# Kernel optimization log

Hardware: AMD Instinct MI355X
Metric: run time of the kernel (lower is better)

## Reference

```python
import jax, jax.numpy as jnp
import numpy as np

GRID = 4
N = GRID * GRID  # 16 nodes
CIN = 16
HID = 64
HEADS = 4
OUT = 256
NEG_SLOPE = 0.2  # PyG GATConv default leaky relu slope
LN_EPS = 1e-5


def _adj_mask():
    # 4-connected grid adjacency + self loops (PyG GATConv add_self_loops=True)
    m = np.zeros((N, N), dtype=bool)
    for i in range(GRID):
        for j in range(GRID):
            u = i * GRID + j
            if j + 1 < GRID:
                v = i * GRID + j + 1
                m[u, v] = m[v, u] = True
            if i + 1 < GRID:
                v = (i + 1) * GRID + j
                m[u, v] = m[v, u] = True
    np.fill_diagonal(m, True)
    return m

ADJ = jnp.asarray(_adj_mask())  # [N, N], adj[i, j] = j is a (self-)neighbor of i


def gat_layer(h, W, a_src, a_dst, b, concat):
    """PyG GATConv on the fixed grid graph, dense-masked form.
    h: [B, N, Fin]; W: [Fin, HEADS*C]; a_src/a_dst: [HEADS, C]."""
    B = h.shape[0]
    H, C = a_src.shape
    wh = (h @ W).reshape(B, N, H, C)                       # [B, N, H, C]
    e_src = jnp.einsum('bnhc,hc->bnh', wh, a_src)          # alpha_src . Wh_j
    e_dst = jnp.einsum('bnhc,hc->bnh', wh, a_dst)          # alpha_dst . Wh_i
    # score[b, i, j, h]: target i attends to source j
    e = e_dst[:, :, None, :] + e_src[:, None, :, :]
    e = jax.nn.leaky_relu(e, NEG_SLOPE)
    e = jnp.where(ADJ[None, :, :, None], e, -1e9)
    alpha = jax.nn.softmax(e, axis=2)                      # softmax over sources j
    out = jnp.einsum('bijh,bjhc->bihc', alpha, wh)         # [B, N, H, C]
    if concat:
        out = out.reshape(B, N, H * C)
    else:
        out = out.mean(axis=2)
    return out + b


def setup_inputs() -> dict:
    key = jax.random.key(0)
    ks = jax.random.split(key, 24)
    s = 0.05
    B = 16384
    inp = {
        'x': jax.random.normal(ks[0], (B, CIN, GRID, GRID), dtype=jnp.float32),
        'w_in': jax.random.normal(ks[1], (CIN, HID), dtype=jnp.float32) * s,
        'b_in': jnp.zeros((HID,), jnp.float32),
        # GAT layer 0: in 64 -> 4 heads x 64, concat
        'W0': jax.random.normal(ks[2], (HID, HEADS * HID), dtype=jnp.float32) * s,
        'asrc0': jax.random.normal(ks[3], (HEADS, HID), dtype=jnp.float32) * s,
        'adst0': jax.random.normal(ks[4], (HEADS, HID), dtype=jnp.float32) * s,
        'bb0': jnp.zeros((HEADS * HID,), jnp.float32),
        # GAT layer 1: in 256 -> 4 heads x 64, concat
        'W1': jax.random.normal(ks[5], (HEADS * HID, HEADS * HID), dtype=jnp.float32) * s,
        'asrc1': jax.random.normal(ks[6], (HEADS, HID), dtype=jnp.float32) * s,
        'adst1': jax.random.normal(ks[7], (HEADS, HID), dtype=jnp.float32) * s,
        'bb1': jnp.zeros((HEADS * HID,), jnp.float32),
        # GAT layer 2: in 256 -> 4 heads x 64, mean over heads (concat=False)
        'W2': jax.random.normal(ks[8], (HEADS * HID, HEADS * HID), dtype=jnp.float32) * s,
        'asrc2': jax.random.normal(ks[9], (HEADS, HID), dtype=jnp.float32) * s,
        'adst2': jax.random.normal(ks[10], (HEADS, HID), dtype=jnp.float32) * s,
        'bb2': jnp.zeros((HID,), jnp.float32),
        # output MLP: 64 -> 128 (LN, ReLU) -> 256
        'w1': jax.random.normal(ks[11], (HID, OUT // 2), dtype=jnp.float32) * s,
        'b1': jnp.zeros((OUT // 2,), jnp.float32),
        'ln_g': jnp.ones((OUT // 2,), jnp.float32),
        'ln_b': jnp.zeros((OUT // 2,), jnp.float32),
        'w2': jax.random.normal(ks[12], (OUT // 2, OUT), dtype=jnp.float32) * s,
        'b2': jnp.zeros((OUT,), jnp.float32),
    }
    return inp


def reference(x, w_in, b_in, W0, asrc0, adst0, bb0, W1, asrc1, adst1, bb1,
              W2, asrc2, adst2, bb2, w1, b1, ln_g, ln_b, w2, b2):
    B = x.shape[0]
    # grid_to_graph: (B, C, H, W) -> (B, N, C) node features
    h = jnp.transpose(x, (0, 2, 3, 1)).reshape(B, N, CIN)
    h = jax.nn.relu(h @ w_in + b_in)
    h = gat_layer(h, W0, asrc0, adst0, bb0, concat=True)
    h = jax.nn.relu(h)  # dropout is identity at inference
    h = gat_layer(h, W1, asrc1, adst1, bb1, concat=True)
    h = jax.nn.relu(h)
    h = gat_layer(h, W2, asrc2, adst2, bb2, concat=False)  # [B, N, 64]
    g = h.mean(axis=1)  # global_mean_pool over the 16 nodes of each graph
    # MLP with LayerNorm
    y = g @ w1 + b1
    mu = y.mean(axis=-1, keepdims=True)
    var = ((y - mu) ** 2).mean(axis=-1, keepdims=True)
    y = (y - mu) * jax.lax.rsqrt(var + LN_EPS) * ln_g + ln_b
    y = jax.nn.relu(y)
    return y @ w2 + b2
```

## Files before the change

### kernel.cpp

```cpp
#include <hip/hip_runtime.h>
#include <hip/hip_bf16.h>

typedef short s8v __attribute__((ext_vector_type(8)));
typedef short s4v __attribute__((ext_vector_type(4)));
typedef float f4v __attribute__((ext_vector_type(4)));

#define WSTR 36
#define AP   20

#define HIXBASE(s, quad) (((s)*4 + (quad))*256)

__device__ constexpr unsigned KMASK[16] = {
  0x0013u,0x0027u,0x004Eu,0x008Cu,
  0x0131u,0x0272u,0x04E4u,0x08C8u,
  0x1310u,0x2720u,0x4E40u,0x8C80u,
  0x3100u,0x7200u,0xE400u,0xC800u};

__device__ __forceinline__ short f2b(float x){
  __hip_bfloat16 h = __float2bfloat16(x);
  return *reinterpret_cast<short*>(&h);
}
__device__ __forceinline__ float b2f(short s){
  __hip_bfloat16 h = *reinterpret_cast<__hip_bfloat16*>(&s);
  return __bfloat162float(h);
}
__device__ __forceinline__ unsigned pk2(float a, float b){
  unsigned ua = __float_as_uint(a), ub = __float_as_uint(b);
  ua += 0x7fffu + ((ua >> 16) & 1u);
  ub += 0x7fffu + ((ub >> 16) & 1u);
  return __builtin_amdgcn_perm(ub, ua, 0x07060302);
}

__global__ __launch_bounds__(256) void prep_all(
  const float* __restrict__ W0, const float* __restrict__ as0, const float* __restrict__ ad0,
  const float* __restrict__ W1, const float* __restrict__ as1, const float* __restrict__ ad1,
  const float* __restrict__ W2, const float* __restrict__ as2, const float* __restrict__ ad2,
  const float* __restrict__ w_in,
  short* __restrict__ ws)
{
  short* WPin = ws;
  short* WP0  = ws + 2048;
  short* WP1  = ws + 2048 + 17408;
  short* WP2  = ws + 2048 + 17408 + 69632;

  const int t = threadIdx.x, l = t & 63;
  const int gid = blockIdx.x*4 + (t >> 6);

  if (gid < 288){
    const float* W; short* WP; int u = gid, f, s, KS;
    if (u < 32)      { W = W0; WP = WP0; KS = 2; f = u >> 1; s = u & 1; }
    else if (u < 160){ u -= 32;  W = W1; WP = WP1; KS = 8; f = u >> 3; s = u & 7; }
    else             { u -= 160; W = W2; WP = WP2; KS = 8; f = u >> 3; s = u & 7; }
    const int lq = l & 15, quad = l >> 4;
    union { s8v v; short s16[8]; } o;
    #pragma unroll
    for (int j = 0; j < 8; ++j)
      o.s16[j] = f2b(W[(s*32 + quad*8 + j)*256 + f*16 + lq]);
    *(s8v*)(WP + ((f*KS + s)*64 + l)*8) = o.v;
  } else if (gid < 292){
    const int f = gid - 288;
    const int lq = l & 15, quad = l >> 4;
    union { s8v v; short s16[8]; } o;
    #pragma unroll
    for (int j = 0; j < 8; ++j){
      const int k = quad*8 + j;
      o.s16[j] = (k < 16) ? f2b(w_in[k*64 + f*16 + lq]) : (short)0;
    }
    *(s8v*)(WPin + (f*64 + l)*8) = o.v;
  } else {
    int u = gid - 292;
    const float* W; const float* as; const float* ad; short* WP; int KS, k;
    if (u < 64)      { W=W0; as=as0; ad=ad0; WP=WP0; KS=2; k=u; }
    else if (u < 320){ u-=64;  W=W1; as=as1; ad=ad1; WP=WP1; KS=8; k=u; }
    else             { u-=320; W=W2; as=as2; ad=ad2; WP=WP2; KS=8; k=u; }
    float v[8];
    #pragma unroll
    for (int h = 0; h < 4; ++h){
      const float wv_ = W[k*256 + h*64 + l];
      v[h]   = wv_ * as[h*64 + l];
      v[4+h] = wv_ * ad[h*64 + l];
    }
    #pragma unroll
    for (int s = 1; s < 64; s <<= 1)
      #pragma unroll
      for (int uu = 0; uu < 8; ++uu) v[uu] += __shfl_xor(v[uu], s, 64);
    if (l < 16){
      const float r = (l < 8) ? v[l] : 0.f;
      WP[((16*KS + (k >> 5))*64 + ((k >> 3) & 3)*16 + l)*8 + (k & 7)] = f2b(r);
    }
  }
}

template<int KS, bool MEAN>
__device__ __forceinline__ void gat_layer(short* bufH, short* whT, short* alphaS,
    const short* __restrict__ WP, const float* __restrict__ bbias,
    float* gsm, const int t)
{
  const int l = t & 63, wv = t >> 6, lq = l & 15, quad = l >> 4;
  {
    f4v acc[5][2];
    #pragma unroll
    for (int fi = 0; fi < 5; ++fi)
      #pragma unroll
      for (int nt = 0; nt < 2; ++nt) acc[fi][nt] = (f4v){0.f,0.f,0.f,0.f};
    #pragma unroll
    for (int s = 0; s < KS; ++s){
      const s8v a0 = *(const s8v*)&bufH[HIXBASE(s, quad) + lq*8];
      const s8v a1 = *(const s8v*)&bufH[HIXBASE(s, quad) + (16 + lq)*8];
      #pragma unroll
      for (int fi = 0; fi < 5; ++fi){
        if (fi == 4 && wv != 3) break;
        const int f = (fi == 4) ? 16 : fi*4 + wv;
        const s8v bF = *(const s8v*)&WP[((f*KS + s)*64 + l)*8];
        acc[fi][0] = __builtin_amdgcn_mfma_f32_16x16x32_bf16(a0, bF, acc[fi][0], 0,0,0);
        acc[fi][1] = __builtin_amdgcn_mfma_f32_16x16x32_bf16(a1, bF, acc[fi][1], 0,0,0);
      }
    }
    #pragma unroll
    for (int fi = 0; fi < 5; ++fi){
      if (fi == 4 && (wv != 3 || lq >= 8)) break;
      const int f = (fi == 4) ? 16 : fi*4 + wv;
      #pragma unroll
      for (int nt = 0; nt < 2; ++nt){
        uint2 p;
        p.x = pk2(acc[fi][nt][0], acc[fi][nt][1]);
        p.y = pk2(acc[fi][nt][2], acc[fi][nt][3]);
        *(uint2*)&whT[(f*16 + lq)*WSTR + nt*16 + quad*4] = p;
      }
    }
  }
  __syncthreads();
  if (t < 128){
    const int g = t >> 6, h = (t >> 4) & 3, i = t & 15;
    const float ed = b2f(whT[(260 + h)*WSTR + g*16 + i]);
    float ev[16];
    #pragma unroll
    for (int c = 0; c < 4; ++c){
      const s4v v = *(const s4v*)&whT[(256 + h)*WSTR + g*16 + c*4];
      ev[c*4+0]=b2f(v[0]); ev[c*4+1]=b2f(v[1]); ev[c*4+2]=b2f(v[2]); ev[c*4+3]=b2f(v[3]);
    }
    const unsigned m = KMASK[i];
    float ssum = 0.f;
    #pragma unroll
    for (int j = 0; j < 16; ++j){
      float e = ed + ev[j];
      e = (e > 0.f) ? e : 0.2f*e;
      const float a = ((m >> j) & 1u) ? __expf(e) : 0.f;
      ev[j] = a; ssum += a;
    }
    const float inv = 1.f / ssum;
    unsigned* row = (unsigned*)&alphaS[((g*4 + h)*16 + i)*AP];
    #pragma unroll
    for (int c = 0; c < 8; ++c)
      row[c] = pk2(ev[2*c]*inv, ev[2*c+1]*inv);
  }
  __syncthreads();
  if constexpr (!MEAN){
    const int h = wv;
    union { s8v v; unsigned u[4]; } B[2];
    #pragma unroll
    for (int g = 0; g < 2; ++g){
      const unsigned* ar = (const unsigned*)&alphaS[((g*4 + h)*16 + lq)*AP + (quad & 1)*8];
      const bool act = ((quad >> 1) == g);
      #pragma unroll
      for (int c = 0; c < 4; ++c) B[g].u[c] = act ? ar[c] : 0u;
    }
    #pragma unroll
    for (int ct = 0; ct < 4; ++ct){
      const s8v a = *(const s8v*)&whT[(h*64 + ct*16 + lq)*WSTR + quad*8];
      const int sf = h*2 + (ct >> 1);
      const int qf = (ct & 1)*2 + (quad >> 1);
      const int jf = (quad & 1)*4;
      const int f0 = h*64 + ct*16 + quad*4;
      const float4 bb = *(const float4*)&bbias[f0];
      #pragma unroll
      for (int g = 0; g < 2; ++g){
        f4v d = (f4v){0.f,0.f,0.f,0.f};
        d = __builtin_amdgcn_mfma_f32_16x16x32_bf16(a, B[g].v, d, 0,0,0);
        uint2 p;
        p.x = pk2(fmaxf(d[0] + bb.x, 0.f), fmaxf(d[1] + bb.y, 0.f));
        p.y = pk2(fmaxf(d[2] + bb.z, 0.f), fmaxf(d[3] + bb.w, 0.f));
        *(uint2*)&bufH[HIXBASE(sf, qf) + (g*16 + lq)*8 + jf] = p;
      }
    }
  } else {
    const int g = wv >> 1;
    union { s8v v; unsigned u[4]; } B[4];
    #pragma unroll
    for (int h = 0; h < 4; ++h){
      const unsigned* ar = (const unsigned*)&alphaS[((g*4 + h)*16 + lq)*AP + (quad & 1)*8];
      const bool act = ((quad >> 1) == g);
      #pragma unroll
      for (int c = 0; c < 4; ++c) B[h].u[c] = act ? ar[c] : 0u;
    }
    #pragma unroll
    for (int cc = 0; cc < 2; ++cc){
      const int ct = (wv & 1)*2 + cc;
      f4v d = (f4v){0.f,0.f,0.f,0.f};
      #pragma unroll
      for (int h = 0; h < 4; ++h){
        const s8v a = *(const s8v*)&whT[(h*64 + ct*16 + lq)*WSTR + quad*8];
        d = __builtin_amdgcn_mfma_f32_16x16x32_bf16(a, B[h].v, d, 0,0,0);
      }
      #pragma unroll
      for (int s = 1; s < 16; s <<= 1){
        d[0] += __shfl_xor(d[0], s, 64); d[1] += __shfl_xor(d[1], s, 64);
        d[2] += __shfl_xor(d[2], s, 64); d[3] += __shfl_xor(d[3], s, 64);
      }
      if (lq == 0){
        const int f0 = ct*16 + quad*4;
        const float4 bb = *(const float4*)&bbias[f0];
        float4 gv;
        gv.x = d[0]*(1.f/64.f) + bb.x; gv.y = d[1]*(1.f/64.f) + bb.y;
        gv.z = d[2]*(1.f/64.f) + bb.z; gv.w = d[3]*(1.f/64.f) + bb.w;
        *(float4*)&gsm[g*64 + f0] = gv;
      }
    }
  }
}

__global__ __launch_bounds__(256, 4) void gat_main(
  const float* __restrict__ x,
  const short* __restrict__ WPin, const float* __restrict__ b_in,
  const short* __restrict__ WP0,  const float* __restrict__ bb0,
  const short* __restrict__ WP1,  const float* __restrict__ bb1,
  const short* __restrict__ WP2,  const float* __restrict__ bb2,
  const float* __restrict__ w1,   const float* __restrict__ b1,
  const float* __restrict__ lng,  const float* __restrict__ lnb,
  const float* __restrict__ w2,   const float* __restrict__ b2,
  float* __restrict__ out)
{
  __shared__ __align__(16) short smem[8*4*32*8 + 264*WSTR + 8*16*AP];
  short* bufH   = smem;
  short* whT    = smem + 8192;
  short* alphaS = smem + 8192 + 264*WSTR;
  short* h0   = whT;
  float* gsm  = (float*)bufH;
  float* ylds = gsm + 128;
  float* red  = ylds + 256;
  constexpr int H0S = 40;

  const int b = blockIdx.x;
  const int t = threadIdx.x;
  const int l = t & 63, wv = t >> 6, lq = l & 15, quad = l >> 4;

  {
    const float2 v = *(const float2*)&x[b*512 + 2*t];
    const int i0 = 2*t;
    const int g = i0 >> 8, c = (i0 >> 4) & 15, n = i0 & 15;
    h0[(g*16 + n)*H0S + c]     = f2b(v.x);
    h0[(g*16 + n + 1)*H0S + c] = f2b(v.y);
    const int r = t >> 3, cc = 16 + 2*(t & 7);
    h0[r*H0S + cc] = 0; h0[r*H0S + cc + 1] = 0;
  }
  __syncthreads();

  {
    const s8v aF  = *(const s8v*)&WPin[(wv*64 + l)*8];
    const s8v b0v = *(const s8v*)&h0[lq*H0S + quad*8];
    const s8v b1v = *(const s8v*)&h0[(16+lq)*H0S + quad*8];
    f4v acc0 = (f4v){0.f,0.f,0.f,0.f}, acc1 = (f4v){0.f,0.f,0.f,0.f};
    acc0 = __builtin_amdgcn_mfma_f32_16x16x32_bf16(aF, b0v, acc0, 0,0,0);
    acc1 = __builtin_amdgcn_mfma_f32_16x16x32_bf16(aF, b1v, acc1, 0,0,0);
    const int f0 = wv*16 + quad*4;
    const float4 bi = *(const float4*)&b_in[f0];
    const int sf = wv >> 1;
    const int qf = (wv & 1)*2 + (quad >> 1);
    const int jf = (quad & 1)*4;
    uint2 p0, p1;
    p0.x = pk2(fmaxf(acc0[0]+bi.x,0.f), fmaxf(acc0[1]+bi.y,0.f));
    p0.y = pk2(fmaxf(acc0[2]+bi.z,0.f), fmaxf(acc0[3]+bi.w,0.f));
    p1.x = pk2(fmaxf(acc1[0]+bi.x,0.f), fmaxf(acc1[1]+bi.y,0.f));
    p1.y = pk2(fmaxf(acc1[2]+bi.z,0.f), fmaxf(acc1[3]+bi.w,0.f));
    *(uint2*)&bufH[HIXBASE(sf, qf) + lq*8 + jf]        = p0;
    *(uint2*)&bufH[HIXBASE(sf, qf) + (16 + lq)*8 + jf] = p1;
  }
  __syncthreads();

  gat_layer<2, false>(bufH, whT, alphaS, WP0, bb0, gsm, t);
  __syncthreads();
  gat_layer<8, false>(bufH, whT, alphaS, WP1, bb1, gsm, t);
  __syncthreads();
  gat_layer<8, true >(bufH, whT, alphaS, WP2, bb2, gsm, t);
  __syncthreads();

  const int gg = t >> 7, o = t & 127;
  float yv = b1[o];
  #pragma unroll 8
  for (int k = 0; k < 64; ++k) yv += gsm[gg*64 + k] * w1[k*128 + o];
  float s1 = yv, s2 = yv*yv;
  #pragma unroll
  for (int s = 1; s < 64; s <<= 1){ s1 += __shfl_xor(s1, s, 64); s2 += __shfl_xor(s2, s, 64); }
  if ((t & 63) == 0){ red[(t>>6)*2] = s1; red[(t>>6)*2 + 1] = s2; }
  __syncthreads();
  {
    const float S1 = red[4*gg] + red[4*gg+2], S2 = red[4*gg+1] + red[4*gg+3];
    const float mu  = S1 * (1.f/128.f);
    const float var = S2 * (1.f/128.f) - mu*mu;
    const float yn  = (yv - mu) * rsqrtf(var + 1e-5f) * lng[o] + lnb[o];
    ylds[gg*128 + o] = fmaxf(yn, 0.f);
  }
  __syncthreads();
  float a0 = b2[t], a1 = b2[t];
  #pragma unroll 4
  for (int k = 0; k < 128; ++k){
    const float wv2 = w2[k*256 + t];
    a0 += ylds[k]*wv2; a1 += ylds[128 + k]*wv2;
  }
  out[(b*2 + 0)*256 + t] = a0;
  out[(b*2 + 1)*256 + t] = a1;
}

extern "C" void kernel_launch(void* const* d_in, const int* in_sizes, int n_in,
                              void* d_out, int out_size, void* d_ws, size_t ws_size,
                              hipStream_t stream){
  const float* x    = (const float*)d_in[0];
  const float* w_in = (const float*)d_in[1];
  const float* b_in = (const float*)d_in[2];
  const float* W0   = (const float*)d_in[3];
  const float* as0  = (const float*)d_in[4];
  const float* ad0  = (const float*)d_in[5];
  const float* bb0  = (const float*)d_in[6];
  const float* W1   = (const float*)d_in[7];
  const float* as1  = (const float*)d_in[8];
  const float* ad1  = (const float*)d_in[9];
  const float* bb1  = (const float*)d_in[10];
  const float* W2   = (const float*)d_in[11];
  const float* as2  = (const float*)d_in[12];
  const float* ad2  = (const float*)d_in[13];
  const float* bb2  = (const float*)d_in[14];
  const float* w1   = (const float*)d_in[15];
  const float* b1   = (const float*)d_in[16];
  const float* lng  = (const float*)d_in[17];
  const float* lnb  = (const float*)d_in[18];
  const float* w2   = (const float*)d_in[19];
  const float* b2   = (const float*)d_in[20];
  const int B = in_sizes[0] / 256;

  short* ws = (short*)d_ws;
  const short* WPin = ws;
  const short* WP0  = ws + 2048;
  const short* WP1  = ws + 2048 + 17408;
  const short* WP2  = ws + 2048 + 17408 + 69632;

  prep_all<<<217, 256, 0, stream>>>(W0, as0, ad0, W1, as1, ad1, W2, as2, ad2,
                                    w_in, ws);
  gat_main<<<B/2, 256, 0, stream>>>(x, WPin, b_in, WP0, bb0, WP1, bb1, WP2, bb2,
                                    w1, b1, lng, lnb, w2, b2, (float*)d_out);
}
```

Measured before the change: 330.2 us.

## Process four graphs per block with 512 threads to reuse weight fragments

Each block now handles four graphs (64 node rows) with eight waves instead of two graphs with four waves. In the projection GEMM each wave loads two weight B-fragments per K step and applies them to all four node tiles, so weight traffic per graph is halved. The attention, aggregation, mean-pool, LayerNorm and output MLP stages are reindexed for four graphs, with whT widened and shared buffers doubled. In exchange, LDS per block roughly doubles and the block is larger, which may limit how many blocks fit on a CU and increase register pressure.

After: 559.6 us. 69.5% more time.

```diff
diff --git a/kernel.cpp b/kernel.cpp
--- a/kernel.cpp
+++ b/kernel.cpp
@@ -5,10 +5,9 @@
 typedef short s4v __attribute__((ext_vector_type(4)));
 typedef float f4v __attribute__((ext_vector_type(4)));
 
-#define WSTR 36
+#define WSTR 68
 #define AP   20
-
-#define HIXBASE(s, quad) (((s)*4 + (quad))*256)
+#define HIX(s, quad) (((s)*4 + (quad))*512)
 
 __device__ constexpr unsigned KMASK[16] = {
   0x0013u,0x0027u,0x004Eu,0x008Cu,
@@ -98,39 +97,47 @@
 {
   const int l = t & 63, wv = t >> 6, lq = l & 15, quad = l >> 4;
   {
-    f4v acc[5][2];
-    #pragma unroll
-    for (int fi = 0; fi < 5; ++fi)
-      #pragma unroll
-      for (int nt = 0; nt < 2; ++nt) acc[fi][nt] = (f4v){0.f,0.f,0.f,0.f};
+    f4v acc0[4], acc1[4], acc2;
+    #pragma unroll
+    for (int nt = 0; nt < 4; ++nt){
+      acc0[nt] = (f4v){0.f,0.f,0.f,0.f};
+      acc1[nt] = (f4v){0.f,0.f,0.f,0.f};
+    }
+    acc2 = (f4v){0.f,0.f,0.f,0.f};
     #pragma unroll
     for (int s = 0; s < KS; ++s){
-      const s8v a0 = *(const s8v*)&bufH[HIXBASE(s, quad) + lq*8];
-      const s8v a1 = *(const s8v*)&bufH[HIXBASE(s, quad) + (16 + lq)*8];
-      #pragma unroll
-      for (int fi = 0; fi < 5; ++fi){
-        if (fi == 4 && wv != 3) break;
-        const int f = (fi == 4) ? 16 : fi*4 + wv;
-        const s8v bF = *(const s8v*)&WP[((f*KS + s)*64 + l)*8];
-        acc[fi][0] = __builtin_amdgcn_mfma_f32_16x16x32_bf16(a0, bF, acc[fi][0], 0,0,0);
-        acc[fi][1] = __builtin_amdgcn_mfma_f32_16x16x32_bf16(a1, bF, acc[fi][1], 0,0,0);
-      }
-    }
-    #pragma unroll
-    for (int fi = 0; fi < 5; ++fi){
-      if (fi == 4 && (wv != 3 || lq >= 8)) break;
-      const int f = (fi == 4) ? 16 : fi*4 + wv;
-      #pragma unroll
-      for (int nt = 0; nt < 2; ++nt){
-        uint2 p;
-        p.x = pk2(acc[fi][nt][0], acc[fi][nt][1]);
-        p.y = pk2(acc[fi][nt][2], acc[fi][nt][3]);
-        *(uint2*)&whT[(f*16 + lq)*WSTR + nt*16 + quad*4] = p;
-      }
-    }
-  }
-  __syncthreads();
-  if (t < 128){
+      s8v a[4];
+      #pragma unroll
+      for (int nt = 0; nt < 4; ++nt)
+        a[nt] = *(const s8v*)&bufH[HIX(s, quad) + (nt*16 + lq)*8];
+      const s8v b0 = *(const s8v*)&WP[((wv*KS + s)*64 + l)*8];
+      const s8v b1 = *(const s8v*)&WP[(((wv + 8)*KS + s)*64 + l)*8];
+      #pragma unroll
+      for (int nt = 0; nt < 4; ++nt){
+        acc0[nt] = __builtin_amdgcn_mfma_f32_16x16x32_bf16(a[nt], b0, acc0[nt], 0,0,0);
+        acc1[nt] = __builtin_amdgcn_mfma_f32_16x16x32_bf16(a[nt], b1, acc1[nt], 0,0,0);
+      }
+      if (wv >= 4){
+        const s8v b2 = *(const s8v*)&WP[((16*KS + s)*64 + l)*8];
+        acc2 = __builtin_amdgcn_mfma_f32_16x16x32_bf16(a[wv - 4], b2, acc2, 0,0,0);
+      }
+    }
+    #pragma unroll
+    for (int nt = 0; nt < 4; ++nt){
+      uint2 p;
+      p.x = pk2(acc0[nt][0], acc0[nt][1]); p.y = pk2(acc0[nt][2], acc0[nt][3]);
+      *(uint2*)&whT[(wv*16 + lq)*WSTR + nt*16 + quad*4] = p;
+      p.x = pk2(acc1[nt][0], acc1[nt][1]); p.y = pk2(acc1[nt][2], acc1[nt][3]);
+      *(uint2*)&whT[((wv + 8)*16 + lq)*WSTR + nt*16 + quad*4] = p;
+    }
+    if (wv >= 4 && lq < 8){
+      uint2 p;
+      p.x = pk2(acc2[0], acc2[1]); p.y = pk2(acc2[2], acc2[3]);
+      *(uint2*)&whT[(256 + lq)*WSTR + (wv - 4)*16 + quad*4] = p;
+    }
+  }
+  __syncthreads();
+  if (t < 256){
     const int g = t >> 6, h = (t >> 4) & 3, i = t & 15;
     const float ed = b2f(whT[(260 + h)*WSTR + g*16 + i]);
     float ev[16];
@@ -156,51 +163,52 @@
   }
   __syncthreads();
   if constexpr (!MEAN){
-    const int h = wv;
-    union { s8v v; unsigned u[4]; } B[2];
-    #pragma unroll
-    for (int g = 0; g < 2; ++g){
-      const unsigned* ar = (const unsigned*)&alphaS[((g*4 + h)*16 + lq)*AP + (quad & 1)*8];
-      const bool act = ((quad >> 1) == g);
-      #pragma unroll
-      for (int c = 0; c < 4; ++c) B[g].u[c] = act ? ar[c] : 0u;
+    const int h = wv & 3, gp = wv >> 2;
+    union { s8v v; unsigned u[4]; } Bv[2];
+    #pragma unroll
+    for (int gi = 0; gi < 2; ++gi){
+      const int gg = gp*2 + gi;
+      const unsigned* ar = (const unsigned*)&alphaS[((gg*4 + h)*16 + lq)*AP + (quad & 1)*8];
+      const bool act = ((quad >> 1) == gi);
+      #pragma unroll
+      for (int c = 0; c < 4; ++c) Bv[gi].u[c] = act ? ar[c] : 0u;
     }
     #pragma unroll
     for (int ct = 0; ct < 4; ++ct){
-      const s8v a = *(const s8v*)&whT[(h*64 + ct*16 + lq)*WSTR + quad*8];
+      const s8v a = *(const s8v*)&whT[(h*64 + ct*16 + lq)*WSTR + gp*32 + quad*8];
+      const int f0 = h*64 + ct*16 + quad*4;
+      const float4 bb = *(const float4*)&bbias[f0];
       const int sf = h*2 + (ct >> 1);
       const int qf = (ct & 1)*2 + (quad >> 1);
       const int jf = (quad & 1)*4;
-      const int f0 = h*64 + ct*16 + quad*4;
-      const float4 bb = *(const float4*)&bbias[f0];
-      #pragma unroll
-      for (int g = 0; g < 2; ++g){
+      #pragma unroll
+      for (int gi = 0; gi < 2; ++gi){
         f4v d = (f4v){0.f,0.f,0.f,0.f};
-        d = __builtin_amdgcn_mfma_f32_16x16x32_bf16(a, B[g].v, d, 0,0,0);
+        d = __builtin_amdgcn_mfma_f32_16x16x32_bf16(a, Bv[gi].v, d, 0,0,0);
         uint2 p;
         p.x = pk2(fmaxf(d[0] + bb.x, 0.f), fmaxf(d[1] + bb.y, 0.f));
         p.y = pk2(fmaxf(d[2] + bb.z, 0.f), fmaxf(d[3] + bb.w, 0.f));
-        *(uint2*)&bufH[HIXBASE(sf, qf) + (g*16 + lq)*8 + jf] = p;
+        *(uint2*)&bufH[HIX(sf, qf) + ((gp*2 + gi)*16 + lq)*8 + jf] = p;
       }
     }
   } else {
-    const int g = wv >> 1;
-    union { s8v v; unsigned u[4]; } B[4];
+    const int g = wv >> 1, ctp = wv & 1;
+    union { s8v v; unsigned u[4]; } Bv[4];
     #pragma unroll
     for (int h = 0; h < 4; ++h){
       const unsigned* ar = (const unsigned*)&alphaS[((g*4 + h)*16 + lq)*AP + (quad & 1)*8];
-      const bool act = ((quad >> 1) == g);
-      #pragma unroll
-      for (int c = 0; c < 4; ++c) B[h].u[c] = act ? ar[c] : 0u;
+      const bool act = ((quad >> 1) == (g & 1));
+      #pragma unroll
+      for (int c = 0; c < 4; ++c) Bv[h].u[c] = act ? ar[c] : 0u;
     }
     #pragma unroll
     for (int cc = 0; cc < 2; ++cc){
-      const int ct = (wv & 1)*2 + cc;
+      const int ct = ctp*2 + cc;
       f4v d = (f4v){0.f,0.f,0.f,0.f};
       #pragma unroll
       for (int h = 0; h < 4; ++h){
-        const s8v a = *(const s8v*)&whT[(h*64 + ct*16 + lq)*WSTR + quad*8];
-        d = __builtin_amdgcn_mfma_f32_16x16x32_bf16(a, B[h].v, d, 0,0,0);
+        const s8v a = *(const s8v*)&whT[(h*64 + ct*16 + lq)*WSTR + (g >> 1)*32 + quad*8];
+        d = __builtin_amdgcn_mfma_f32_16x16x32_bf16(a, Bv[h].v, d, 0,0,0);
       }
       #pragma unroll
       for (int s = 1; s < 16; s <<= 1){
@@ -219,7 +227,7 @@
   }
 }
 
-__global__ __launch_bounds__(256, 4) void gat_main(
+__global__ __launch_bounds__(512, 4) void gat_main(
   const float* __restrict__ x,
   const short* __restrict__ WPin, const float* __restrict__ b_in,
   const short* __restrict__ WP0,  const float* __restrict__ bb0,
@@ -230,14 +238,14 @@
   const float* __restrict__ w2,   const float* __restrict__ b2,
   float* __restrict__ out)
 {
-  __shared__ __align__(16) short smem[8*4*32*8 + 264*WSTR + 8*16*AP];
+  __shared__ __align__(16) short smem[16384 + 264*WSTR + 16*16*AP];
   short* bufH   = smem;
-  short* whT    = smem + 8192;
-  short* alphaS = smem + 8192 + 264*WSTR;
+  short* whT    = smem + 16384;
+  short* alphaS = smem + 16384 + 264*WSTR;
   short* h0   = whT;
   float* gsm  = (float*)bufH;
-  float* ylds = gsm + 128;
-  float* red  = ylds + 256;
+  float* ylds = gsm + 256;
+  float* red  = gsm + 768;
   constexpr int H0S = 40;
 
   const int b = blockIdx.x;
@@ -245,7 +253,7 @@
   const int l = t & 63, wv = t >> 6, lq = l & 15, quad = l >> 4;
 
   {
-    const float2 v = *(const float2*)&x[b*512 + 2*t];
+    const float2 v = *(const float2*)&x[(size_t)b*1024 + 2*t];
     const int i0 = 2*t;
     const int g = i0 >> 8, c = (i0 >> 4) & 15, n = i0 & 15;
     h0[(g*16 + n)*H0S + c]     = f2b(v.x);
@@ -256,24 +264,24 @@
   __syncthreads();
 
   {
-    const s8v aF  = *(const s8v*)&WPin[(wv*64 + l)*8];
-    const s8v b0v = *(const s8v*)&h0[lq*H0S + quad*8];
-    const s8v b1v = *(const s8v*)&h0[(16+lq)*H0S + quad*8];
-    f4v acc0 = (f4v){0.f,0.f,0.f,0.f}, acc1 = (f4v){0.f,0.f,0.f,0.f};
-    acc0 = __builtin_amdgcn_mfma_f32_16x16x32_bf16(aF, b0v, acc0, 0,0,0);
-    acc1 = __builtin_amdgcn_mfma_f32_16x16x32_bf16(aF, b1v, acc1, 0,0,0);
-    const int f0 = wv*16 + quad*4;
+    const int ft = wv >> 1, ntp = wv & 1;
+    const s8v aF = *(const s8v*)&WPin[(ft*64 + l)*8];
+    const int f0 = ft*16 + quad*4;
     const float4 bi = *(const float4*)&b_in[f0];
-    const int sf = wv >> 1;
-    const int qf = (wv & 1)*2 + (quad >> 1);
+    const int sf = ft >> 1;
+    const int qf = (ft & 1)*2 + (quad >> 1);
     const int jf = (quad & 1)*4;
-    uint2 p0, p1;
-    p0.x = pk2(fmaxf(acc0[0]+bi.x,0.f), fmaxf(acc0[1]+bi.y,0.f));
-    p0.y = pk2(fmaxf(acc0[2]+bi.z,0.f), fmaxf(acc0[3]+bi.w,0.f));
-    p1.x = pk2(fmaxf(acc1[0]+bi.x,0.f), fmaxf(acc1[1]+bi.y,0.f));
-    p1.y = pk2(fmaxf(acc1[2]+bi.z,0.f), fmaxf(acc1[3]+bi.w,0.f));
-    *(uint2*)&bufH[HIXBASE(sf, qf) + lq*8 + jf]        = p0;
-    *(uint2*)&bufH[HIXBASE(sf, qf) + (16 + lq)*8 + jf] = p1;
+    #pragma unroll
+    for (int ni = 0; ni < 2; ++ni){
+      const int nt = ntp*2 + ni;
+      const s8v bv = *(const s8v*)&h0[(nt*16 + lq)*H0S + quad*8];
+      f4v acc = (f4v){0.f,0.f,0.f,0.f};
+      acc = __builtin_amdgcn_mfma_f32_16x16x32_bf16(aF, bv, acc, 0,0,0);
+      uint2 p;
+      p.x = pk2(fmaxf(acc[0]+bi.x,0.f), fmaxf(acc[1]+bi.y,0.f));
+      p.y = pk2(fmaxf(acc[2]+bi.z,0.f), fmaxf(acc[3]+bi.w,0.f));
+      *(uint2*)&bufH[HIX(sf, qf) + (nt*16 + lq)*8 + jf] = p;
+    }
   }
   __syncthreads();
 
@@ -284,31 +292,34 @@
   gat_layer<8, true >(bufH, whT, alphaS, WP2, bb2, gsm, t);
   __syncthreads();
 
-  const int gg = t >> 7, o = t & 127;
-  float yv = b1[o];
+  const int gy = t >> 7, oy = t & 127;
+  float yv = b1[oy];
   #pragma unroll 8
-  for (int k = 0; k < 64; ++k) yv += gsm[gg*64 + k] * w1[k*128 + o];
+  for (int k = 0; k < 64; ++k) yv += gsm[gy*64 + k] * w1[k*128 + oy];
   float s1 = yv, s2 = yv*yv;
   #pragma unroll
   for (int s = 1; s < 64; s <<= 1){ s1 += __shfl_xor(s1, s, 64); s2 += __shfl_xor(s2, s, 64); }
   if ((t & 63) == 0){ red[(t>>6)*2] = s1; red[(t>>6)*2 + 1] = s2; }
   __syncthreads();
   {
-    const float S1 = red[4*gg] + red[4*gg+2], S2 = red[4*gg+1] + red[4*gg+3];
+    const float S1 = red[4*gy] + red[4*gy+2], S2 = red[4*gy+1] + red[4*gy+3];
     const float mu  = S1 * (1.f/128.f);
     const float var = S2 * (1.f/128.f) - mu*mu;
-    const float yn  = (yv - mu) * rsqrtf(var + 1e-5f) * lng[o] + lnb[o];
-    ylds[gg*128 + o] = fmaxf(yn, 0.f);
-  }
-  __syncthreads();
-  float a0 = b2[t], a1 = b2[t];
-  #pragma unroll 4
-  for (int k = 0; k < 128; ++k){
-    const float wv2 = w2[k*256 + t];
-    a0 += ylds[k]*wv2; a1 += ylds[128 + k]*wv2;
-  }
-  out[(b*2 + 0)*256 + t] = a0;
-  out[(b*2 + 1)*256 + t] = a1;
+    const float yn  = (yv - mu) * rsqrtf(var + 1e-5f) * lng[oy] + lnb[oy];
+    ylds[gy*128 + oy] = fmaxf(yn, 0.f);
+  }
+  __syncthreads();
+  {
+    const int oo = t & 255, g2 = (t >> 8)*2;
+    float a0 = b2[oo], a1 = b2[oo];
+    #pragma unroll 4
+    for (int k = 0; k < 128; ++k){
+      const float wv2 = w2[k*256 + oo];
+      a0 += ylds[g2*128 + k]*wv2; a1 += ylds[(g2+1)*128 + k]*wv2;
+    }
+    out[((size_t)b*4 + g2)*256 + oo]     = a0;
+    out[((size_t)b*4 + g2 + 1)*256 + oo] = a1;
+  }
 }
 
 extern "C" void kernel_launch(void* const* d_in, const int* in_sizes, int n_in,
@@ -345,6 +356,6 @@
 
   prep_all<<<217, 256, 0, stream>>>(W0, as0, ad0, W1, as1, ad1, W2, as2, ad2,
                                     w_in, ws);
-  gat_main<<<B/2, 256, 0, stream>>>(x, WPin, b_in, WP0, bb0, WP1, bb1, WP2, bb2,
+  gat_main<<<B/4, 512, 0, stream>>>(x, WPin, b_in, WP0, bb0, WP1, bb1, WP2, bb2,
                                     w1, b1, lng, lnb, w2, b2, (float*)d_out);
 }
```

## Split MLP tail into separate kernel using output buffer as scratch

Applied to the files above, without the earlier changes.

Splits the fused kernel in two. The GAT layers now write pooled features into the output buffer, and a new mlp_tail kernel runs the LayerNorm MLP, reading those features back and overwriting each block's output region in place. The aim is to lighten the main kernel's registers and code so more GAT blocks fit per CU, and to run the tail at higher occupancy. In exchange it adds a kernel launch and a global round trip for the pooled features. Correctness relies on each tail block finishing its reads before its own writes, which the in-block syncthreads ensures.

Result: no change. 336.6 us (+1.9%).

```diff
diff --git a/kernel.cpp b/kernel.cpp
--- a/kernel.cpp
+++ b/kernel.cpp
@@ -7,7 +7,6 @@
 
 #define WSTR 36
 #define AP   20
-
 #define HIXBASE(s, quad) (((s)*4 + (quad))*256)
 
 __device__ constexpr unsigned KMASK[16] = {
@@ -94,7 +93,7 @@
 template<int KS, bool MEAN>
 __device__ __forceinline__ void gat_layer(short* bufH, short* whT, short* alphaS,
     const short* __restrict__ WP, const float* __restrict__ bbias,
-    float* gsm, const int t)
+    float* __restrict__ out, const int b, const int t)
 {
   const int l = t & 63, wv = t >> 6, lq = l & 15, quad = l >> 4;
   {
@@ -213,7 +212,7 @@
         float4 gv;
         gv.x = d[0]*(1.f/64.f) + bb.x; gv.y = d[1]*(1.f/64.f) + bb.y;
         gv.z = d[2]*(1.f/64.f) + bb.z; gv.w = d[3]*(1.f/64.f) + bb.w;
-        *(float4*)&gsm[g*64 + f0] = gv;
+        *(float4*)&out[((size_t)b*2 + g)*256 + f0] = gv;
       }
     }
   }
@@ -225,19 +224,13 @@
   const short* __restrict__ WP0,  const float* __restrict__ bb0,
   const short* __restrict__ WP1,  const float* __restrict__ bb1,
   const short* __restrict__ WP2,  const float* __restrict__ bb2,
-  const float* __restrict__ w1,   const float* __restrict__ b1,
-  const float* __restrict__ lng,  const float* __restrict__ lnb,
-  const float* __restrict__ w2,   const float* __restrict__ b2,
   float* __restrict__ out)
 {
   __shared__ __align__(16) short smem[8*4*32*8 + 264*WSTR + 8*16*AP];
   short* bufH   = smem;
   short* whT    = smem + 8192;
   short* alphaS = smem + 8192 + 264*WSTR;
-  short* h0   = whT;
-  float* gsm  = (float*)bufH;
-  float* ylds = gsm + 128;
-  float* red  = ylds + 256;
+  short* h0     = whT;
   constexpr int H0S = 40;
 
   const int b = blockIdx.x;
@@ -277,17 +270,29 @@
   }
   __syncthreads();
 
-  gat_layer<2, false>(bufH, whT, alphaS, WP0, bb0, gsm, t);
-  __syncthreads();
-  gat_layer<8, false>(bufH, whT, alphaS, WP1, bb1, gsm, t);
-  __syncthreads();
-  gat_layer<8, true >(bufH, whT, alphaS, WP2, bb2, gsm, t);
-  __syncthreads();
-
+  gat_layer<2, false>(bufH, whT, alphaS, WP0, bb0, out, b, t);
+  __syncthreads();
+  gat_layer<8, false>(bufH, whT, alphaS, WP1, bb1, out, b, t);
+  __syncthreads();
+  gat_layer<8, true >(bufH, whT, alphaS, WP2, bb2, out, b, t);
+}
+
+__global__ __launch_bounds__(256, 8) void mlp_tail(
+  const float* __restrict__ w1,  const float* __restrict__ b1,
+  const float* __restrict__ lng, const float* __restrict__ lnb,
+  const float* __restrict__ w2,  const float* __restrict__ b2,
+  float* __restrict__ out)
+{
+  __shared__ float ylds[256];
+  __shared__ float red[8];
+  const int b = blockIdx.x;
+  const int t = threadIdx.x;
   const int gg = t >> 7, o = t & 127;
+  const float* gptr = out + ((size_t)b*2 + gg)*256;
+
   float yv = b1[o];
   #pragma unroll 8
-  for (int k = 0; k < 64; ++k) yv += gsm[gg*64 + k] * w1[k*128 + o];
+  for (int k = 0; k < 64; ++k) yv += gptr[k] * w1[k*128 + o];
   float s1 = yv, s2 = yv*yv;
   #pragma unroll
   for (int s = 1; s < 64; s <<= 1){ s1 += __shfl_xor(s1, s, 64); s2 += __shfl_xor(s2, s, 64); }
@@ -307,8 +312,8 @@
     const float wv2 = w2[k*256 + t];
     a0 += ylds[k]*wv2; a1 += ylds[128 + k]*wv2;
   }
-  out[(b*2 + 0)*256 + t] = a0;
-  out[(b*2 + 1)*256 + t] = a1;
+  out[((size_t)b*2 + 0)*256 + t] = a0;
+  out[((size_t)b*2 + 1)*256 + t] = a1;
 }
 
 extern "C" void kernel_launch(void* const* d_in, const int* in_sizes, int n_in,
@@ -346,5 +351,6 @@
   prep_all<<<217, 256, 0, stream>>>(W0, as0, ad0, W1, as1, ad1, W2, as2, ad2,
                                     w_in, ws);
   gat_main<<<B/2, 256, 0, stream>>>(x, WPin, b_in, WP0, bb0, WP1, bb1, WP2, bb2,
-                                    w1, b1, lng, lnb, w2, b2, (float*)d_out);
-}
+                                    (float*)d_out);
+  mlp_tail<<<B/2, 256, 0, stream>>>(w1, b1, lng, lnb, w2, b2, (float*)d_out);
+}
```
